# Optimization experiments

Hardware: AMD Instinct MI355X
Metric: run time of the kernel (lower is better)

Reference implementation:

```python
import jax, jax.numpy as jnp
import numpy as np

N, E, DIN, H, HEADS = 50000, 800000, 128, 64, 4


def setup_inputs() -> dict:
    key = jax.random.key(0)
    ks = jax.random.split(key, 12)

    def p(k, shape, fan_in):
        return jax.random.normal(k, shape, dtype=jnp.float32) / np.float32(np.sqrt(fan_in))

    return dict(
        x=jax.random.normal(ks[0], (N, DIN), dtype=jnp.float32),
        edge_index=jax.random.randint(ks[1], (2, E), 0, N, dtype=jnp.int32),
        # GCNConv(input_dim, hidden)
        W_gcn=p(ks[2], (DIN, H), DIN), b_gcn=jnp.zeros((H,), jnp.float32),
        # GATConv(hidden, hidden, heads=4, concat=True)
        W_gat=p(ks[3], (H, HEADS * H), H),
        att_src=p(ks[4], (HEADS, H), H), att_dst=p(ks[5], (HEADS, H), H),
        b_gat=jnp.zeros((HEADS * H,), jnp.float32),
        # SAGEConv(4*hidden, hidden): lin_l (neighbors, with bias), lin_r (root, no bias)
        W_sage_l=p(ks[6], (HEADS * H, H), HEADS * H), b_sage=jnp.zeros((H,), jnp.float32),
        W_sage_r=p(ks[7], (HEADS * H, H), HEADS * H),
        # edge-pair MLP: Linear(2*hidden, hidden) -> ReLU -> Linear(hidden, 1)
        W1=p(ks[8], (2 * H, H), 2 * H), b1=jnp.zeros((H,), jnp.float32),
        W2=p(ks[9], (H, 1), H), b2=jnp.zeros((1,), jnp.float32),
    )


def reference(x, edge_index, W_gcn, b_gcn, W_gat, att_src, att_dst, b_gat,
              W_sage_l, b_sage, W_sage_r, W1, b1, W2, b2):
    n = x.shape[0]
    src, dst = edge_index[0], edge_index[1]
    loop = jnp.arange(n, dtype=edge_index.dtype)
    # edges with self-loops appended (GCN and GAT add self-loops by default)
    s2 = jnp.concatenate([src, loop])
    d2 = jnp.concatenate([dst, loop])

    h = x @ W_gcn                                            # [N, H]
    deg = jax.ops.segment_sum(jnp.ones_like(d2, jnp.float32), d2, num_segments=n)
    dinv = jnp.where(deg > 0, jax.lax.rsqrt(jnp.maximum(deg, 1e-12)), 0.0)
    norm = dinv[s2] * dinv[d2]                               # [E+N]
    h = jax.ops.segment_sum(h[s2] * norm[:, None], d2, num_segments=n) + b_gcn
    h = jax.nn.relu(h)                                       # dropout: identity in eval

    # ---- GATConv (heads=4, concat=True, negative_slope=0.2) ----
    g = (h @ W_gat).reshape(n, HEADS, H)                     # [N, heads, C]
    a_s = jnp.sum(g * att_src, axis=-1)                      # [N, heads]
    a_d = jnp.sum(g * att_dst, axis=-1)
    e = jax.nn.leaky_relu(a_s[s2] + a_d[d2], 0.2)            # [E+N, heads]
    m = jax.ops.segment_max(e, d2, num_segments=n)           # per-target max (stable softmax)
    e = jnp.exp(e - m[d2])
    z = jax.ops.segment_sum(e, d2, num_segments=n)
    alpha = e / (z[d2] + 1e-16)                              # edge softmax over incoming edges
    g = jax.ops.segment_sum(g[s2] * alpha[:, :, None], d2, num_segments=n)
    g = jax.nn.relu(g.reshape(n, HEADS * H) + b_gat)

    # ---- SAGEConv (mean aggregation, root weight, no self-loops) ----
    nsum = jax.ops.segment_sum(g[src], dst, num_segments=n)
    cnt = jax.ops.segment_sum(jnp.ones_like(dst, jnp.float32), dst, num_segments=n)
    mean = nsum / jnp.maximum(cnt, 1.0)[:, None]
    s = jax.nn.relu(mean @ W_sage_l + b_sage + g @ W_sage_r)  # [N, H]

    # ---- edge-pair MLP + sigmoid ----
    ef = jnp.concatenate([s[src], s[dst]], axis=1)            # [E, 2H]
    pred = jax.nn.relu(ef @ W1 + b1) @ W2 + b2                # [E, 1]
    return jax.nn.sigmoid(pred[:, 0])
```

## Files before the change

### kernel.cpp

```cpp
#include <hip/hip_runtime.h>
#include <math.h>

typedef float v2f __attribute__((ext_vector_type(2)));
static __device__ __forceinline__ float4 f4s(float v){ return make_float4(v,v,v,v); }
static __device__ __forceinline__ float4 f4add(float4 a, float4 b){ return make_float4(a.x+b.x,a.y+b.y,a.z+b.z,a.w+b.w); }
static __device__ __forceinline__ float4 f4max(float4 a, float4 b){ return make_float4(fmaxf(a.x,b.x),fmaxf(a.y,b.y),fmaxf(a.z,b.z),fmaxf(a.w,b.w)); }
static __device__ __forceinline__ float4 f4scale(float4 a, float s){ return make_float4(a.x*s,a.y*s,a.z*s,a.w*s); }
static __device__ __forceinline__ float4 f4fma(float4 acc, float s, float4 b){
  acc.x += s*b.x; acc.y += s*b.y; acc.z += s*b.z; acc.w += s*b.w; return acc;
}
static __device__ __forceinline__ float4 f4relu(float4 a){ return f4max(a, f4s(0.f)); }
static __device__ __forceinline__ float4 f4leaky(float4 a){
  return make_float4(a.x>0.f?a.x:0.2f*a.x, a.y>0.f?a.y:0.2f*a.y, a.z>0.f?a.z:0.2f*a.z, a.w>0.f?a.w:0.2f*a.w);
}
static __device__ __forceinline__ float4 f4expf(float4 a){ return make_float4(__expf(a.x),__expf(a.y),__expf(a.z),__expf(a.w)); }
static __device__ __forceinline__ unsigned short f2bf(float f){
  unsigned int u = __float_as_uint(f);
  unsigned int r = (u + 0x7fffu + ((u >> 16) & 1u)) >> 16;
  return (unsigned short)r;
}
static __device__ __forceinline__ ushort4 f2bf4(float4 f){
  ushort4 r; r.x=f2bf(f.x); r.y=f2bf(f.y); r.z=f2bf(f.z); r.w=f2bf(f.w); return r;
}
static __device__ __forceinline__ float4 bfu2f4(uint2 u){
  return make_float4(__uint_as_float(u.x << 16), __uint_as_float(u.x & 0xffff0000u),
                     __uint_as_float(u.y << 16), __uint_as_float(u.y & 0xffff0000u));
}
static __device__ __forceinline__ float4 bfu2f4_lo(uint4 u){ return bfu2f4(make_uint2(u.x, u.y)); }
static __device__ __forceinline__ float4 bfu2f4_hi(uint4 u){ return bfu2f4(make_uint2(u.z, u.w)); }

typedef __attribute__((ext_vector_type(8))) unsigned short u16x8;
static __device__ __forceinline__ u16x8 f2bf8(float4 a, float4 b){
  u16x8 r;
  r[0]=f2bf(a.x); r[1]=f2bf(a.y); r[2]=f2bf(a.z); r[3]=f2bf(a.w);
  r[4]=f2bf(b.x); r[5]=f2bf(b.y); r[6]=f2bf(b.z); r[7]=f2bf(b.w);
  return r;
}
static __device__ __forceinline__ void red2(float4& a, float4& b){
  a.x += __shfl_xor(a.x, 8); a.y += __shfl_xor(a.y, 8);
  a.z += __shfl_xor(a.z, 8); a.w += __shfl_xor(a.w, 8);
  b.x += __shfl_xor(b.x, 8); b.y += __shfl_xor(b.y, 8);
  b.z += __shfl_xor(b.z, 8); b.w += __shfl_xor(b.w, 8);
}
static __device__ __forceinline__ unsigned char f2fp8(float v){
  return (unsigned char)(__builtin_amdgcn_cvt_pk_fp8_f32(v, v, 0, false) & 0xff);
}
static __device__ __forceinline__ unsigned int f4_fp8x4(float4 v){
  unsigned int r = __builtin_amdgcn_cvt_pk_fp8_f32(v.x, v.y, 0, false);
  r = __builtin_amdgcn_cvt_pk_fp8_f32(v.z, v.w, r, true);
  return r;
}
static __device__ __forceinline__ float4 fp8x4_f4(unsigned int q){
  v2f lo = __builtin_amdgcn_cvt_pk_f32_fp8(q, false);
  v2f hi = __builtin_amdgcn_cvt_pk_f32_fp8(q, true);
  return make_float4(lo[0], lo[1], hi[0], hi[1]);
}
static __device__ __forceinline__ float dot8(float4 a, float4 b, const float* v){
  return a.x*v[0]+a.y*v[1]+a.z*v[2]+a.w*v[3]+b.x*v[4]+b.y*v[5]+b.z*v[6]+b.w*v[7];
}

typedef __attribute__((ext_vector_type(8))) short bf16x8;
typedef __attribute__((ext_vector_type(4))) float f32x4;

__global__ __launch_bounds__(256) void k_rankw(const int* __restrict__ dst, int* __restrict__ cnt,
                                               int* __restrict__ rank, int E, int fb,
                                               const float* __restrict__ Wg, const float* __restrict__ Wl,
                                               const float* __restrict__ Wr, unsigned short* __restrict__ WT){
  if ((int)blockIdx.x < fb){
    int t = blockIdx.x*256 + threadIdx.x;
    if (t < E) rank[t] = atomicAdd(&cnt[dst[t]], 1);
    return;
  }
  int s = (blockIdx.x - fb)*256 + threadIdx.x;
  int l = s & 63, f = s >> 6;
  const float* wp; int ld;
  if (s < 2048){
    int cc = f & 15, kb = f >> 4;
    int c  = cc*16 + (l & 15);
    int kr = kb*32 + ((l >> 4) << 3);
    wp = Wg + (size_t)kr*256 + c; ld = 256;
  } else {
    int f2 = f - 32;
    int cc = f2 & 7, kb = f2 >> 3;
    int c  = cc*16 + (l & 15);
    int kr = kb*32 + ((l >> 4) << 3);
    wp = (c >= 64) ? (Wr + (size_t)kr*64 + (c - 64)) : (Wl + (size_t)kr*64 + c);
    ld = 64;
  }
  u16x8 o;
  #pragma unroll
  for (int j = 0; j < 8; ++j) o[j] = f2bf(wp[(size_t)j*ld]);
  *(u16x8*)(WT + (size_t)s*8) = o;
}

__global__ __launch_bounds__(256) void k_scan1v(const int* __restrict__ cnt, int* __restrict__ excl,
                                                int* __restrict__ bsum, int n, int nb,
                                                const float* __restrict__ Wg, const float* __restrict__ as,
                                                const float* __restrict__ ad, float* __restrict__ Vs,
                                                float* __restrict__ Vd){
  if ((int)blockIdx.x == nb){
    int t = threadIdx.x;
    int h = t >> 6, k = t & 63;
    float s = 0.f, d = 0.f;
    const float* wr = Wg + (size_t)k*256 + h*64;
    const float* ar = as + h*64;
    const float* dr = ad + h*64;
    for (int c = 0; c < 64; ++c){ float w = wr[c]; s += w*ar[c]; d += w*dr[c]; }
    Vs[t] = s; Vd[t] = d;
    return;
  }
  __shared__ int sc[256];
  int t = threadIdx.x; int i = blockIdx.x*256 + t;
  int v = (i<n)?cnt[i]:0;
  sc[t]=v; __syncthreads();
  for (int o=1;o<256;o<<=1){ int a=(t>=o)?sc[t-o]:0; __syncthreads(); sc[t]+=a; __syncthreads(); }
  if (i<n) excl[i] = sc[t]-v;
  if (t==255) bsum[blockIdx.x] = sc[t];
}
__global__ __launch_bounds__(256) void k_scan3b(const int* __restrict__ cnt, const int* __restrict__ excl,
                                                const int* __restrict__ bsum, int* __restrict__ offs,
                                                float* __restrict__ dinv, int n, int E, int nb){
  __shared__ int sb[256];
  int t = threadIdx.x;
  int v = (t<nb)?bsum[t]:0;
  sb[t]=v; __syncthreads();
  for (int o=1;o<256;o<<=1){ int a=(t>=o)?sb[t-o]:0; __syncthreads(); sb[t]+=a; __syncthreads(); }
  int bex = sb[blockIdx.x] - bsum[blockIdx.x];
  int i = blockIdx.x*256 + t;
  if (i < n){
    offs[i] = excl[i] + bex;
    dinv[i] = rsqrtf((float)cnt[i] + 1.0f);
    if (i == 0) offs[n] = E;
  }
}

__global__ __launch_bounds__(256) void k_fillg(const int* __restrict__ src, const int* __restrict__ dstv,
                                               const int* __restrict__ offs, const int* __restrict__ rank,
                                               int* __restrict__ csr, int E, int fb,
                                               const float* __restrict__ x, const float* __restrict__ Wg,
                                               unsigned char* __restrict__ a8, int n,
                                               const float* __restrict__ dinv){
  if ((int)blockIdx.x < fb){
    int t = blockIdx.x*256 + threadIdx.x;
    if (t < E) csr[offs[dstv[t]] + rank[t]] = src[t];
    return;
  }
  __shared__ unsigned short wb[1024*8];
  int tid = threadIdx.x;
  for (int s = tid; s < 1024; s += 256){
    int l = s & 63, f = s >> 6;
    int cc = f & 3, kb = f >> 2;
    int c  = cc*16 + (l & 15);
    int kr = kb*32 + ((l >> 4) << 3);
    const float* wp = Wg + (size_t)kr*64 + c;
    unsigned short* dp = &wb[s*8];
    #pragma unroll
    for (int j = 0; j < 8; ++j) dp[j] = f2bf(wp[(size_t)j*64]);
  }
  __syncthreads();
  int wv = tid >> 6, l = tid & 63;
  int lrow = l & 15;
  int lk = (l >> 4) << 3;
  int g = blockIdx.x - fb;
  int r0 = (g << 6) + (wv << 4);
  int m = r0 + lrow;
  bf16x8 afr[4];
  #pragma unroll
  for (int kb = 0; kb < 4; ++kb){
    bf16x8 a = {0,0,0,0,0,0,0,0};
    if (m < n){
      const float* p = x + (size_t)m*128 + kb*32 + lk;
      float4 f0 = *(const float4*)p;
      float4 f1 = *(const float4*)(p + 4);
      a[0]=(short)f2bf(f0.x); a[1]=(short)f2bf(f0.y); a[2]=(short)f2bf(f0.z); a[3]=(short)f2bf(f0.w);
      a[4]=(short)f2bf(f1.x); a[5]=(short)f2bf(f1.y); a[6]=(short)f2bf(f1.z); a[7]=(short)f2bf(f1.w);
    }
    afr[kb] = a;
  }
  int rbase = r0 + ((l >> 4) << 2);
  float sc[4];
  #pragma unroll
  for (int r = 0; r < 4; ++r) sc[r] = (rbase + r < n) ? dinv[rbase + r] : 0.f;
  #pragma unroll
  for (int cc = 0; cc < 4; ++cc){
    f32x4 acc = {0.f, 0.f, 0.f, 0.f};
    #pragma unroll
    for (int kb = 0; kb < 4; ++kb){
      bf16x8 b = *(const bf16x8*)&wb[((kb*4 + cc)*64 + l)*8];
      acc = __builtin_amdgcn_mfma_f32_16x16x32_bf16(afr[kb], b, acc, 0, 0, 0);
    }
    int c = cc*16 + lrow;
    #pragma unroll
    for (int r = 0; r < 4; ++r){
      int rr = rbase + r;
      if (rr < n) a8[(size_t)rr*64 + c] = f2fp8(acc[r] * sc[r]);
    }
  }
}

__global__ __launch_bounds__(256, 4) void k_gatsage(const unsigned short* __restrict__ Y,
                                                    const unsigned short* __restrict__ WT,
                                                    const float* __restrict__ bg,
                                                    unsigned short* __restrict__ R,
                                                    unsigned char* __restrict__ P8, int n){
  constexpr int LDG = 264;
  __shared__ unsigned short gb[64*LDG];
  const unsigned short* WT1 = WT;
  const unsigned short* WT2 = WT + 2048*8;
  int tid = threadIdx.x;
  int wv = tid >> 6, l = tid & 63;
  int lrow = l & 15;
  int lk = (l >> 4) << 3;
  int rbase4 = (l >> 4) << 2;
  int r0 = ((int)blockIdx.x << 6) + (wv << 4);
  int m = r0 + lrow;
  bf16x8 afr[4][2];
  #pragma unroll
  for (int h = 0; h < 4; ++h){
    #pragma unroll
    for (int kb = 0; kb < 2; ++kb){
      bf16x8 a = {0,0,0,0,0,0,0,0};
      if (m < n) a = *(const bf16x8*)(Y + (size_t)m*256 + h*64 + kb*32 + lk);
      afr[h][kb] = a;
    }
  }
  #pragma unroll
  for (int cc = 0; cc < 16; ++cc){
    f32x4 acc = {0.f, 0.f, 0.f, 0.f};
    int hh = cc >> 2;
    #pragma unroll
    for (int kb = 0; kb < 2; ++kb){
      bf16x8 b = *(const bf16x8*)&WT1[((size_t)((kb*16 + cc)*64 + l))*8];
      acc = __builtin_amdgcn_mfma_f32_16x16x32_bf16(afr[hh][kb], b, acc, 0, 0, 0);
    }
    int c = cc*16 + lrow;
    float bv = bg[c];
    #pragma unroll
    for (int r = 0; r < 4; ++r){
      int lr = (wv << 4) + rbase4 + r;
      gb[lr*LDG + c] = f2bf(fmaxf(acc[r] + bv, 0.f));
    }
  }
  bf16x8 afb[8];
  #pragma unroll
  for (int kb = 0; kb < 8; ++kb)
    afb[kb] = *(const bf16x8*)&gb[((wv << 4) + lrow)*LDG + kb*32 + lk];
  #pragma unroll
  for (int cc = 0; cc < 8; ++cc){
    f32x4 acc = {0.f, 0.f, 0.f, 0.f};
    #pragma unroll
    for (int kb = 0; kb < 8; ++kb){
      bf16x8 b = *(const bf16x8*)&WT2[((size_t)((kb*8 + cc)*64 + l))*8];
      acc = __builtin_amdgcn_mfma_f32_16x16x32_bf16(afb[kb], b, acc, 0, 0, 0);
    }
    int c = cc*16 + lrow;
    #pragma unroll
    for (int r = 0; r < 4; ++r){
      int rr = r0 + rbase4 + r;
      if (rr < n){
        float v = acc[r];
        if (c < 64) P8[(size_t)rr*64 + c] = f2fp8(v);
        else        R[(size_t)rr*64 + (c - 64)] = f2bf(v);
      }
    }
  }
}

__global__ __launch_bounds__(256) void k_gcn(const unsigned char* __restrict__ a8, const float* __restrict__ dinv,
                                             const float* __restrict__ b, const int* __restrict__ offs,
                                             const int* __restrict__ csr, const float* __restrict__ Vs,
                                             const float* __restrict__ Vd, unsigned char* __restrict__ h8,
                                             float* __restrict__ D, int n){
  __shared__ float svs[256], svd[256];
  svs[threadIdx.x] = Vs[threadIdx.x];
  svd[threadIdx.x] = Vd[threadIdx.x];
  __syncthreads();
  int l = threadIdx.x & 63;
  int node = (((blockIdx.x*256 + threadIdx.x) >> 6) << 2) + (l >> 4);
  int l15 = l & 15;
  int grp = l15 >> 3, sub = l15 & 7;
  bool ok = node < n;
  int beg = 0, end = 0;
  float di = 0.f;
  if (ok){ beg = offs[node]; end = offs[node+1]; di = dinv[node]; }
  float4 aL0 = f4s(0.f), aH0 = f4s(0.f), aL1 = f4s(0.f), aH1 = f4s(0.f);
  int i = beg + grp;
  for (; i + 2 < end; i += 4){
    int s0 = csr[i], s1 = csr[i+2];
    uint2 u0 = *(const uint2*)(a8 + (size_t)s0*64 + (sub<<3));
    uint2 u1 = *(const uint2*)(a8 + (size_t)s1*64 + (sub<<3));
    aL0 = f4add(aL0, fp8x4_f4(u0.x)); aH0 = f4add(aH0, fp8x4_f4(u0.y));
    aL1 = f4add(aL1, fp8x4_f4(u1.x)); aH1 = f4add(aH1, fp8x4_f4(u1.y));
  }
  if (i < end){
    int s0 = csr[i];
    uint2 u0 = *(const uint2*)(a8 + (size_t)s0*64 + (sub<<3));
    aL0 = f4add(aL0, fp8x4_f4(u0.x)); aH0 = f4add(aH0, fp8x4_f4(u0.y));
  }
  float4 aL = f4add(aL0, aL1), aH = f4add(aH0, aH1);
  red2(aL, aH);
  if (ok){
    uint2 us = *(const uint2*)(a8 + (size_t)node*64 + (sub<<3));
    aL = f4add(aL, fp8x4_f4(us.x)); aH = f4add(aH, fp8x4_f4(us.y));
    float4 b0 = *(const float4*)(b + (sub<<3));
    float4 b1 = *(const float4*)(b + (sub<<3) + 4);
    float4 r0 = f4relu(f4fma(b0, di, aL));
    float4 r1 = f4relu(f4fma(b1, di, aH));
    if (grp == 0){
      uint2 q; q.x = f4_fp8x4(r0); q.y = f4_fp8x4(r1);
      *(uint2*)(h8 + (size_t)node*64 + (sub<<3)) = q;
    }
    const float* vs0 = svs + (grp*128) + (sub<<3);
    const float* vd0 = svd + (grp*128) + (sub<<3);
    float s0 = dot8(r0, r1, vs0);
    float s1 = dot8(r0, r1, vs0 + 64);
    float d0 = dot8(r0, r1, vd0);
    float d1 = dot8(r0, r1, vd0 + 64);
    #pragma unroll
    for (int o = 1; o < 8; o <<= 1){
      s0 += __shfl_xor(s0, o); s1 += __shfl_xor(s1, o);
      d0 += __shfl_xor(d0, o); d1 += __shfl_xor(d1, o);
    }
    if (sub == 0){
      *(float2*)(D + (size_t)node*8 + grp*2)     = make_float2(s0, s1);
      *(float2*)(D + (size_t)node*8 + 4 + grp*2) = make_float2(d0, d1);
    }
  }
}

#define GAT_CAP 128
__global__ __launch_bounds__(256) void k_gat2(const float* __restrict__ D, const unsigned char* __restrict__ H8,
                                              const int* __restrict__ offs, const int* __restrict__ csr,
                                              unsigned short* __restrict__ Y, int n){
  __shared__ float wl[8][GAT_CAP*4];
  __shared__ int   sl[8][GAT_CAP];
  int hw = threadIdx.x >> 5;
  int node = (blockIdx.x*256 + threadIdx.x) >> 5;
  int l5 = threadIdx.x & 31;
  if (node >= n) return;
  int beg = offs[node], end = offs[node+1];
  int deg = end - beg;
  float4 ed  = *(const float4*)(D + (size_t)node*8 + 4);
  float4 es0 = *(const float4*)(D + (size_t)node*8);
  float4 wself = f4expf(f4leaky(f4add(es0, ed)));
  float4 z4 = f4s(0.f);
  for (int i = beg + l5; i < end; i += 32){
    int s = csr[i];
    float4 w = f4expf(f4leaky(f4add(*(const float4*)(D + (size_t)s*8), ed)));
    int li = i - beg;
    if (li < GAT_CAP){ *(float4*)&wl[hw][li<<2] = w; sl[hw][li] = s << 6; }
    z4 = f4add(z4, w);
  }
  for (int m = 1; m < 32; m <<= 1){
    z4.x += __shfl_xor(z4.x, m); z4.y += __shfl_xor(z4.y, m);
    z4.z += __shfl_xor(z4.z, m); z4.w += __shfl_xor(z4.w, m);
  }
  z4 = f4add(z4, wself);
  int grp = l5 >> 4;
  int sub = l5 & 15;
  int c0b = sub << 2;
  float4 a0 = f4s(0.f), a1 = f4s(0.f), a2 = f4s(0.f), a3 = f4s(0.f);
  int nl = deg < GAT_CAP ? deg : GAT_CAP;
  int i = grp;
  for (; i + 2 < nl; i += 4){
    int o0 = sl[hw][i], o1 = sl[hw][i+2];
    float4 w0 = *(const float4*)&wl[hw][i<<2];
    float4 w1 = *(const float4*)&wl[hw][(i+2)<<2];
    unsigned int q0 = *(const unsigned int*)(H8 + o0 + c0b);
    unsigned int q1 = *(const unsigned int*)(H8 + o1 + c0b);
    float4 f0 = fp8x4_f4(q0);
    float4 f1 = fp8x4_f4(q1);
    a0 = f4fma(a0, w0.x, f0); a1 = f4fma(a1, w0.y, f0);
    a2 = f4fma(a2, w0.z, f0); a3 = f4fma(a3, w0.w, f0);
    a0 = f4fma(a0, w1.x, f1); a1 = f4fma(a1, w1.y, f1);
    a2 = f4fma(a2, w1.z, f1); a3 = f4fma(a3, w1.w, f1);
  }
  if (i < nl){
    float4 w0 = *(const float4*)&wl[hw][i<<2];
    float4 f0 = fp8x4_f4(*(const unsigned int*)(H8 + sl[hw][i] + c0b));
    a0 = f4fma(a0, w0.x, f0); a1 = f4fma(a1, w0.y, f0);
    a2 = f4fma(a2, w0.z, f0); a3 = f4fma(a3, w0.w, f0);
  }
  for (int j = nl + grp; j < deg; j += 2){
    int s = csr[beg+j];
    float4 e = f4leaky(f4add(*(const float4*)(D + (size_t)s*8), ed));
    float4 w = f4expf(e);
    float4 f0 = fp8x4_f4(*(const unsigned int*)(H8 + ((size_t)s << 6) + c0b));
    a0 = f4fma(a0, w.x, f0); a1 = f4fma(a1, w.y, f0);
    a2 = f4fma(a2, w.z, f0); a3 = f4fma(a3, w.w, f0);
  }
  a0.x += __shfl_xor(a0.x, 16); a0.y += __shfl_xor(a0.y, 16); a0.z += __shfl_xor(a0.z, 16); a0.w += __shfl_xor(a0.w, 16);
  a1.x += __shfl_xor(a1.x, 16); a1.y += __shfl_xor(a1.y, 16); a1.z += __shfl_xor(a1.z, 16); a1.w += __shfl_xor(a1.w, 16);
  a2.x += __shfl_xor(a2.x, 16); a2.y += __shfl_xor(a2.y, 16); a2.z += __shfl_xor(a2.z, 16); a2.w += __shfl_xor(a2.w, 16);
  a3.x += __shfl_xor(a3.x, 16); a3.y += __shfl_xor(a3.y, 16); a3.z += __shfl_xor(a3.z, 16); a3.w += __shfl_xor(a3.w, 16);
  if (grp == 0){
    float4 fs = fp8x4_f4(*(const unsigned int*)(H8 + ((size_t)node << 6) + c0b));
    a0 = f4fma(a0, wself.x, fs);
    a1 = f4fma(a1, wself.y, fs);
    a2 = f4fma(a2, wself.z, fs);
    a3 = f4fma(a3, wself.w, fs);
    a0 = f4scale(a0, 1.f/(z4.x + 1e-16f));
    a1 = f4scale(a1, 1.f/(z4.y + 1e-16f));
    a2 = f4scale(a2, 1.f/(z4.z + 1e-16f));
    a3 = f4scale(a3, 1.f/(z4.w + 1e-16f));
    unsigned short* yp = Y + (size_t)node*256 + (sub << 2);
    *(ushort4*)(yp)       = f2bf4(a0);
    *(ushort4*)(yp + 64)  = f2bf4(a1);
    *(ushort4*)(yp + 128) = f2bf4(a2);
    *(ushort4*)(yp + 192) = f2bf4(a3);
  }
}

__global__ __launch_bounds__(256) void k_sage(const unsigned char* __restrict__ P8, const unsigned short* __restrict__ R,
                                              const float* __restrict__ b, const int* __restrict__ offs,
                                              const int* __restrict__ csr, const float* __restrict__ W1a,
                                              const float* __restrict__ W1b, unsigned char* __restrict__ T2, int n){
  __shared__ unsigned short wfr[1024*8];
  __shared__ unsigned short stile[16][72];
  int tid = threadIdx.x;
  for (int s = tid; s < 1024; s += 256){
    int l = s & 63, f = s >> 6;
    int cc = f & 7, kb = f >> 3;
    int c  = cc*16 + (l & 15);
    int kr = kb*32 + ((l >> 4) << 3);
    const float* wp = (c >= 64) ? (W1b + (size_t)kr*64 + (c - 64)) : (W1a + (size_t)kr*64 + c);
    unsigned short* dp = &wfr[s*8];
    #pragma unroll
    for (int j = 0; j < 8; ++j) dp[j] = f2bf(wp[(size_t)j*64]);
  }
  int wv = tid >> 6, l = tid & 63;
  int base = blockIdx.x*16;
  int lrow16 = (wv << 2) + (l >> 4);
  int node = base + lrow16;
  int l15 = l & 15;
  int grp = l15 >> 3, sub = l15 & 7;
  bool ok = node < n;
  int beg = 0, end = 0;
  if (ok){ beg = offs[node]; end = offs[node+1]; }
  float4 aL0 = f4s(0.f), aH0 = f4s(0.f), aL1 = f4s(0.f), aH1 = f4s(0.f);
  int i = beg + grp;
  for (; i + 2 < end; i += 4){
    int s0 = csr[i], s1 = csr[i+2];
    uint2 u0 = *(const uint2*)(P8 + (size_t)s0*64 + (sub<<3));
    uint2 u1 = *(const uint2*)(P8 + (size_t)s1*64 + (sub<<3));
    aL0 = f4add(aL0, fp8x4_f4(u0.x)); aH0 = f4add(aH0, fp8x4_f4(u0.y));
    aL1 = f4add(aL1, fp8x4_f4(u1.x)); aH1 = f4add(aH1, fp8x4_f4(u1.y));
  }
  if (i < end){
    int s0 = csr[i];
    uint2 u0 = *(const uint2*)(P8 + (size_t)s0*64 + (sub<<3));
    aL0 = f4add(aL0, fp8x4_f4(u0.x)); aH0 = f4add(aH0, fp8x4_f4(u0.y));
  }
  float4 aL = f4add(aL0, aL1), aH = f4add(aH0, aH1);
  red2(aL, aH);
  float4 r0 = f4s(0.f), r1 = f4s(0.f);
  if (ok){
    float minv = 1.f / fmaxf((float)(end - beg), 1.f);
    uint4 ur = *(const uint4*)(R + (size_t)node*64 + (sub<<3));
    float4 b0 = *(const float4*)(b + (sub<<3));
    float4 b1 = *(const float4*)(b + (sub<<3) + 4);
    r0 = f4relu(f4add(f4fma(b0, minv, aL), bfu2f4_lo(ur)));
    r1 = f4relu(f4add(f4fma(b1, minv, aH), bfu2f4_hi(ur)));
  }
  if (grp == 0) *(u16x8*)&stile[lrow16][sub << 3] = f2bf8(r0, r1);
  __syncthreads();
  int lrow = l & 15, lk = (l >> 4) << 3;
  bf16x8 af0 = *(const bf16x8*)&stile[lrow][lk];
  bf16x8 af1 = *(const bf16x8*)&stile[lrow][32 + lk];
  int rbase = (l >> 4) << 2;
  #pragma unroll
  for (int q = 0; q < 2; ++q){
    int cc = wv*2 + q;
    f32x4 acc = {0.f, 0.f, 0.f, 0.f};
    acc = __builtin_amdgcn_mfma_f32_16x16x32_bf16(af0, *(const bf16x8*)&wfr[(cc*64 + l)*8], acc, 0, 0, 0);
    acc = __builtin_amdgcn_mfma_f32_16x16x32_bf16(af1, *(const bf16x8*)&wfr[((8 + cc)*64 + l)*8], acc, 0, 0, 0);
    int c = cc*16 + lrow;
    #pragma unroll
    for (int r = 0; r < 4; ++r){
      int nd = base + rbase + r;
      if (nd < n) T2[(size_t)nd*128 + c] = f2fp8(acc[r]);
    }
  }
}

__global__ __launch_bounds__(256) void k_mlp(const unsigned char* __restrict__ T2,
                                             const float* __restrict__ b1, const float* __restrict__ W2,
                                             const float* __restrict__ b2, const int* __restrict__ src,
                                             const int* __restrict__ dst, float* __restrict__ out, int E){
  int t = threadIdx.x;
  int e = blockIdx.x*32 + (t >> 3);
  if (e >= E) return;
  int sub = t & 7;
  int s = src[e], d = dst[e];
  uint2 uu = *(const uint2*)(T2 + (size_t)s*128 + (sub<<3));
  uint2 vv = *(const uint2*)(T2 + (size_t)d*128 + 64 + (sub<<3));
  float4 u0 = fp8x4_f4(uu.x), u1 = fp8x4_f4(uu.y);
  float4 v0 = fp8x4_f4(vv.x), v1 = fp8x4_f4(vv.y);
  float4 bb0 = *(const float4*)(b1 + (sub<<3));
  float4 bb1 = *(const float4*)(b1 + (sub<<3) + 4);
  float4 w0 = *(const float4*)(W2 + (sub<<3));
  float4 w1 = *(const float4*)(W2 + (sub<<3) + 4);
  float4 ta = f4relu(f4add(f4add(u0, v0), bb0));
  float4 tb = f4relu(f4add(f4add(u1, v1), bb1));
  float p = ta.x*w0.x + ta.y*w0.y + ta.z*w0.z + ta.w*w0.w
          + tb.x*w1.x + tb.y*w1.y + tb.z*w1.z + tb.w*w1.w;
  p += __shfl_xor(p, 1);
  p += __shfl_xor(p, 2);
  p += __shfl_xor(p, 4);
  if (sub == 0) out[e] = 1.f / (1.f + __expf(-(p + b2[0])));
}

extern "C" void kernel_launch(void* const* d_in, const int* in_sizes, int n_in,
                              void* d_out, int out_size, void* d_ws, size_t ws_size,
                              hipStream_t stream){
  const float* x     = (const float*)d_in[0];
  const int*   eidx  = (const int*)  d_in[1];
  const float* W_gcn = (const float*)d_in[2];
  const float* b_gcn = (const float*)d_in[3];
  const float* W_gat = (const float*)d_in[4];
  const float* att_s = (const float*)d_in[5];
  const float* att_d = (const float*)d_in[6];
  const float* b_gat = (const float*)d_in[7];
  const float* W_sl  = (const float*)d_in[8];
  const float* b_sg  = (const float*)d_in[9];
  const float* W_sr  = (const float*)d_in[10];
  const float* W1    = (const float*)d_in[11];
  const float* b1    = (const float*)d_in[12];
  const float* W2    = (const float*)d_in[13];
  const float* b2    = (const float*)d_in[14];
  float* out = (float*)d_out;

  const int N = in_sizes[0] / 128;
  const int E = in_sizes[1] / 2;
  const int* src = eidx;
  const int* dst = eidx + E;

  float* ws   = (float*)d_ws;
  float* dinv = ws;
  float* D    = dinv + (size_t)N;
  float* Vs   = D + (size_t)N*8;
  float* Vd   = Vs + 256;
  unsigned short* WT = (unsigned short*)(Vd + 256);
  unsigned short* Y  = WT + (size_t)6144*8;
  unsigned short* R  = Y + (size_t)N*256;
  unsigned char*  A8 = (unsigned char*)(R + (size_t)N*64);
  unsigned char*  H8 = A8 + (size_t)N*64;
  unsigned char*  P8 = H8 + (size_t)N*64;
  unsigned char*  T2 = P8 + (size_t)N*64;
  int* cnt  = (int*)(T2 + (size_t)N*128);
  int* excl = cnt + N;
  int* bsum = excl + N;
  int* offs = bsum + 256;
  int* rank = offs + N + 1;
  int* csr  = rank + E;

  const int nb = (N + 255) / 256;
  const int fb = (E + 255) / 256;
  const int gtiles = (N + 63) / 64;
  const int nwb = (N + 15) / 16;

  hipMemsetAsync(cnt, 0, (size_t)N*sizeof(int), stream);
  k_rankw <<<fb + 24, 256, 0, stream>>>(dst, cnt, rank, E, fb, W_gat, W_sl, W_sr, WT);
  k_scan1v<<<nb + 1, 256, 0, stream>>>(cnt, excl, bsum, N, nb, W_gat, att_s, att_d, Vs, Vd);
  k_scan3b<<<nb, 256, 0, stream>>>(cnt, excl, bsum, offs, dinv, N, E, nb);
  k_fillg <<<fb + gtiles, 256, 0, stream>>>(src, dst, offs, rank, csr, E, fb,
                                            x, W_gcn, A8, N, dinv);

  k_gcn <<<nwb, 256, 0, stream>>>(A8, dinv, b_gcn, offs, csr, Vs, Vd, H8, D, N);

  k_gat2<<<(N+7)/8, 256, 0, stream>>>(D, H8, offs, csr, Y, N);

  k_gatsage<<<gtiles, 256, 0, stream>>>(Y, WT, b_gat, R, P8, N);

  k_sage<<<nwb, 256, 0, stream>>>(P8, R, b_sg, offs, csr, W1, W1 + 64*64, T2, N);

  k_mlp <<<(E+31)/32, 256, 0, stream>>>(T2, b1, W2, b2, src, dst, out, E);
}
```

Baseline: 276.6 us.

## Fuse GAT aggregation with GAT and SAGE projection matmuls via shared-memory tile

Merges the GAT neighbor aggregation kernel and the follow-on GAT/SAGE projection MFMA kernel into one kernel. Each block aggregates 8 nodes into a 16-row shared-memory tile (upper 8 rows zeroed), then runs both matmuls on that tile and writes P8/R directly. This removes the N×256 bf16 Y round-trip through global memory and one launch. In exchange, half of each 16-row MFMA tile is padding, so matrix work doubles, and the block now carries extra shared memory and barriers, which may lower occupancy.

```diff
diff --git a/kernel.cpp b/kernel.cpp
--- a/kernel.cpp
+++ b/kernel.cpp
@@ -194,74 +194,6 @@
     for (int r = 0; r < 4; ++r){
       int rr = rbase + r;
       if (rr < n) a8[(size_t)rr*64 + c] = f2fp8(acc[r] * sc[r]);
-    }
-  }
-}
-
-__global__ __launch_bounds__(256, 4) void k_gatsage(const unsigned short* __restrict__ Y,
-                                                    const unsigned short* __restrict__ WT,
-                                                    const float* __restrict__ bg,
-                                                    unsigned short* __restrict__ R,
-                                                    unsigned char* __restrict__ P8, int n){
-  constexpr int LDG = 264;
-  __shared__ unsigned short gb[64*LDG];
-  const unsigned short* WT1 = WT;
-  const unsigned short* WT2 = WT + 2048*8;
-  int tid = threadIdx.x;
-  int wv = tid >> 6, l = tid & 63;
-  int lrow = l & 15;
-  int lk = (l >> 4) << 3;
-  int rbase4 = (l >> 4) << 2;
-  int r0 = ((int)blockIdx.x << 6) + (wv << 4);
-  int m = r0 + lrow;
-  bf16x8 afr[4][2];
-  #pragma unroll
-  for (int h = 0; h < 4; ++h){
-    #pragma unroll
-    for (int kb = 0; kb < 2; ++kb){
-      bf16x8 a = {0,0,0,0,0,0,0,0};
-      if (m < n) a = *(const bf16x8*)(Y + (size_t)m*256 + h*64 + kb*32 + lk);
-      afr[h][kb] = a;
-    }
-  }
-  #pragma unroll
-  for (int cc = 0; cc < 16; ++cc){
-    f32x4 acc = {0.f, 0.f, 0.f, 0.f};
-    int hh = cc >> 2;
-    #pragma unroll
-    for (int kb = 0; kb < 2; ++kb){
-      bf16x8 b = *(const bf16x8*)&WT1[((size_t)((kb*16 + cc)*64 + l))*8];
-      acc = __builtin_amdgcn_mfma_f32_16x16x32_bf16(afr[hh][kb], b, acc, 0, 0, 0);
-    }
-    int c = cc*16 + lrow;
-    float bv = bg[c];
-    #pragma unroll
-    for (int r = 0; r < 4; ++r){
-      int lr = (wv << 4) + rbase4 + r;
-      gb[lr*LDG + c] = f2bf(fmaxf(acc[r] + bv, 0.f));
-    }
-  }
-  bf16x8 afb[8];
-  #pragma unroll
-  for (int kb = 0; kb < 8; ++kb)
-    afb[kb] = *(const bf16x8*)&gb[((wv << 4) + lrow)*LDG + kb*32 + lk];
-  #pragma unroll
-  for (int cc = 0; cc < 8; ++cc){
-    f32x4 acc = {0.f, 0.f, 0.f, 0.f};
-    #pragma unroll
-    for (int kb = 0; kb < 8; ++kb){
-      bf16x8 b = *(const bf16x8*)&WT2[((size_t)((kb*8 + cc)*64 + l))*8];
-      acc = __builtin_amdgcn_mfma_f32_16x16x32_bf16(afb[kb], b, acc, 0, 0, 0);
-    }
-    int c = cc*16 + lrow;
-    #pragma unroll
-    for (int r = 0; r < 4; ++r){
-      int rr = r0 + rbase4 + r;
-      if (rr < n){
-        float v = acc[r];
-        if (c < 64) P8[(size_t)rr*64 + c] = f2fp8(v);
-        else        R[(size_t)rr*64 + (c - 64)] = f2bf(v);
-      }
     }
   }
 }
@@ -329,85 +261,147 @@
 }
 
 #define GAT_CAP 128
-__global__ __launch_bounds__(256) void k_gat2(const float* __restrict__ D, const unsigned char* __restrict__ H8,
-                                              const int* __restrict__ offs, const int* __restrict__ csr,
-                                              unsigned short* __restrict__ Y, int n){
+__global__ __launch_bounds__(256) void k_gat2f(const float* __restrict__ D, const unsigned char* __restrict__ H8,
+                                               const int* __restrict__ offs, const int* __restrict__ csr,
+                                               const unsigned short* __restrict__ WT, const float* __restrict__ bg,
+                                               unsigned short* __restrict__ R, unsigned char* __restrict__ P8, int n){
   __shared__ float wl[8][GAT_CAP*4];
   __shared__ int   sl[8][GAT_CAP];
-  int hw = threadIdx.x >> 5;
-  int node = (blockIdx.x*256 + threadIdx.x) >> 5;
-  int l5 = threadIdx.x & 31;
-  if (node >= n) return;
-  int beg = offs[node], end = offs[node+1];
-  int deg = end - beg;
-  float4 ed  = *(const float4*)(D + (size_t)node*8 + 4);
-  float4 es0 = *(const float4*)(D + (size_t)node*8);
-  float4 wself = f4expf(f4leaky(f4add(es0, ed)));
-  float4 z4 = f4s(0.f);
-  for (int i = beg + l5; i < end; i += 32){
-    int s = csr[i];
-    float4 w = f4expf(f4leaky(f4add(*(const float4*)(D + (size_t)s*8), ed)));
-    int li = i - beg;
-    if (li < GAT_CAP){ *(float4*)&wl[hw][li<<2] = w; sl[hw][li] = s << 6; }
-    z4 = f4add(z4, w);
-  }
-  for (int m = 1; m < 32; m <<= 1){
-    z4.x += __shfl_xor(z4.x, m); z4.y += __shfl_xor(z4.y, m);
-    z4.z += __shfl_xor(z4.z, m); z4.w += __shfl_xor(z4.w, m);
-  }
-  z4 = f4add(z4, wself);
+  __shared__ unsigned short ytile[16][264];
+  unsigned short* gtile = (unsigned short*)&wl[0][0];
+  const unsigned short* WT1 = WT;
+  const unsigned short* WT2 = WT + 2048*8;
+  int tid = threadIdx.x;
+  for (int s0 = tid; s0 < 8*264; s0 += 256) (&ytile[8][0])[s0] = 0;
+  int hw = tid >> 5;
+  int node = (blockIdx.x*256 + tid) >> 5;
+  int l5 = tid & 31;
   int grp = l5 >> 4;
   int sub = l5 & 15;
-  int c0b = sub << 2;
-  float4 a0 = f4s(0.f), a1 = f4s(0.f), a2 = f4s(0.f), a3 = f4s(0.f);
-  int nl = deg < GAT_CAP ? deg : GAT_CAP;
-  int i = grp;
-  for (; i + 2 < nl; i += 4){
-    int o0 = sl[hw][i], o1 = sl[hw][i+2];
-    float4 w0 = *(const float4*)&wl[hw][i<<2];
-    float4 w1 = *(const float4*)&wl[hw][(i+2)<<2];
-    unsigned int q0 = *(const unsigned int*)(H8 + o0 + c0b);
-    unsigned int q1 = *(const unsigned int*)(H8 + o1 + c0b);
-    float4 f0 = fp8x4_f4(q0);
-    float4 f1 = fp8x4_f4(q1);
-    a0 = f4fma(a0, w0.x, f0); a1 = f4fma(a1, w0.y, f0);
-    a2 = f4fma(a2, w0.z, f0); a3 = f4fma(a3, w0.w, f0);
-    a0 = f4fma(a0, w1.x, f1); a1 = f4fma(a1, w1.y, f1);
-    a2 = f4fma(a2, w1.z, f1); a3 = f4fma(a3, w1.w, f1);
-  }
-  if (i < nl){
-    float4 w0 = *(const float4*)&wl[hw][i<<2];
-    float4 f0 = fp8x4_f4(*(const unsigned int*)(H8 + sl[hw][i] + c0b));
-    a0 = f4fma(a0, w0.x, f0); a1 = f4fma(a1, w0.y, f0);
-    a2 = f4fma(a2, w0.z, f0); a3 = f4fma(a3, w0.w, f0);
-  }
-  for (int j = nl + grp; j < deg; j += 2){
-    int s = csr[beg+j];
-    float4 e = f4leaky(f4add(*(const float4*)(D + (size_t)s*8), ed));
-    float4 w = f4expf(e);
-    float4 f0 = fp8x4_f4(*(const unsigned int*)(H8 + ((size_t)s << 6) + c0b));
-    a0 = f4fma(a0, w.x, f0); a1 = f4fma(a1, w.y, f0);
-    a2 = f4fma(a2, w.z, f0); a3 = f4fma(a3, w.w, f0);
-  }
-  a0.x += __shfl_xor(a0.x, 16); a0.y += __shfl_xor(a0.y, 16); a0.z += __shfl_xor(a0.z, 16); a0.w += __shfl_xor(a0.w, 16);
-  a1.x += __shfl_xor(a1.x, 16); a1.y += __shfl_xor(a1.y, 16); a1.z += __shfl_xor(a1.z, 16); a1.w += __shfl_xor(a1.w, 16);
-  a2.x += __shfl_xor(a2.x, 16); a2.y += __shfl_xor(a2.y, 16); a2.z += __shfl_xor(a2.z, 16); a2.w += __shfl_xor(a2.w, 16);
-  a3.x += __shfl_xor(a3.x, 16); a3.y += __shfl_xor(a3.y, 16); a3.z += __shfl_xor(a3.z, 16); a3.w += __shfl_xor(a3.w, 16);
-  if (grp == 0){
-    float4 fs = fp8x4_f4(*(const unsigned int*)(H8 + ((size_t)node << 6) + c0b));
-    a0 = f4fma(a0, wself.x, fs);
-    a1 = f4fma(a1, wself.y, fs);
-    a2 = f4fma(a2, wself.z, fs);
-    a3 = f4fma(a3, wself.w, fs);
-    a0 = f4scale(a0, 1.f/(z4.x + 1e-16f));
-    a1 = f4scale(a1, 1.f/(z4.y + 1e-16f));
-    a2 = f4scale(a2, 1.f/(z4.z + 1e-16f));
-    a3 = f4scale(a3, 1.f/(z4.w + 1e-16f));
-    unsigned short* yp = Y + (size_t)node*256 + (sub << 2);
-    *(ushort4*)(yp)       = f2bf4(a0);
-    *(ushort4*)(yp + 64)  = f2bf4(a1);
-    *(ushort4*)(yp + 128) = f2bf4(a2);
-    *(ushort4*)(yp + 192) = f2bf4(a3);
+  if (node < n){
+    int beg = offs[node], end = offs[node+1];
+    int deg = end - beg;
+    float4 ed  = *(const float4*)(D + (size_t)node*8 + 4);
+    float4 es0 = *(const float4*)(D + (size_t)node*8);
+    float4 wself = f4expf(f4leaky(f4add(es0, ed)));
+    float4 z4 = f4s(0.f);
+    for (int i = beg + l5; i < end; i += 32){
+      int s = csr[i];
+      float4 w = f4expf(f4leaky(f4add(*(const float4*)(D + (size_t)s*8), ed)));
+      int li = i - beg;
+      if (li < GAT_CAP){ *(float4*)&wl[hw][li<<2] = w; sl[hw][li] = s << 6; }
+      z4 = f4add(z4, w);
+    }
+    for (int m = 1; m < 32; m <<= 1){
+      z4.x += __shfl_xor(z4.x, m); z4.y += __shfl_xor(z4.y, m);
+      z4.z += __shfl_xor(z4.z, m); z4.w += __shfl_xor(z4.w, m);
+    }
+    z4 = f4add(z4, wself);
+    int c0b = sub << 2;
+    float4 a0 = f4s(0.f), a1 = f4s(0.f), a2 = f4s(0.f), a3 = f4s(0.f);
+    int nl = deg < GAT_CAP ? deg : GAT_CAP;
+    int i = grp;
+    for (; i + 2 < nl; i += 4){
+      int o0 = sl[hw][i], o1 = sl[hw][i+2];
+      float4 w0 = *(const float4*)&wl[hw][i<<2];
+      float4 w1 = *(const float4*)&wl[hw][(i+2)<<2];
+      unsigned int q0 = *(const unsigned int*)(H8 + o0 + c0b);
+      unsigned int q1 = *(const unsigned int*)(H8 + o1 + c0b);
+      float4 f0 = fp8x4_f4(q0);
+      float4 f1 = fp8x4_f4(q1);
+      a0 = f4fma(a0, w0.x, f0); a1 = f4fma(a1, w0.y, f0);
+      a2 = f4fma(a2, w0.z, f0); a3 = f4fma(a3, w0.w, f0);
+      a0 = f4fma(a0, w1.x, f1); a1 = f4fma(a1, w1.y, f1);
+      a2 = f4fma(a2, w1.z, f1); a3 = f4fma(a3, w1.w, f1);
+    }
+    if (i < nl){
+      float4 w0 = *(const float4*)&wl[hw][i<<2];
+      float4 f0 = fp8x4_f4(*(const unsigned int*)(H8 + sl[hw][i] + c0b));
+      a0 = f4fma(a0, w0.x, f0); a1 = f4fma(a1, w0.y, f0);
+      a2 = f4fma(a2, w0.z, f0); a3 = f4fma(a3, w0.w, f0);
+    }
+    for (int j = nl + grp; j < deg; j += 2){
+      int s = csr[beg+j];
+      float4 e = f4leaky(f4add(*(const float4*)(D + (size_t)s*8), ed));
+      float4 w = f4expf(e);
+      float4 f0 = fp8x4_f4(*(const unsigned int*)(H8 + ((size_t)s << 6) + c0b));
+      a0 = f4fma(a0, w.x, f0); a1 = f4fma(a1, w.y, f0);
+      a2 = f4fma(a2, w.z, f0); a3 = f4fma(a3, w.w, f0);
+    }
+    a0.x += __shfl_xor(a0.x, 16); a0.y += __shfl_xor(a0.y, 16); a0.z += __shfl_xor(a0.z, 16); a0.w += __shfl_xor(a0.w, 16);
+    a1.x += __shfl_xor(a1.x, 16); a1.y += __shfl_xor(a1.y, 16); a1.z += __shfl_xor(a1.z, 16); a1.w += __shfl_xor(a1.w, 16);
+    a2.x += __shfl_xor(a2.x, 16); a2.y += __shfl_xor(a2.y, 16); a2.z += __shfl_xor(a2.z, 16); a2.w += __shfl_xor(a2.w, 16);
+    a3.x += __shfl_xor(a3.x, 16); a3.y += __shfl_xor(a3.y, 16); a3.z += __shfl_xor(a3.z, 16); a3.w += __shfl_xor(a3.w, 16);
+    if (grp == 0){
+      float4 fs = fp8x4_f4(*(const unsigned int*)(H8 + ((size_t)node << 6) + c0b));
+      a0 = f4fma(a0, wself.x, fs);
+      a1 = f4fma(a1, wself.y, fs);
+      a2 = f4fma(a2, wself.z, fs);
+      a3 = f4fma(a3, wself.w, fs);
+      a0 = f4scale(a0, 1.f/(z4.x + 1e-16f));
+      a1 = f4scale(a1, 1.f/(z4.y + 1e-16f));
+      a2 = f4scale(a2, 1.f/(z4.z + 1e-16f));
+      a3 = f4scale(a3, 1.f/(z4.w + 1e-16f));
+      unsigned short* yp = &ytile[hw][sub << 2];
+      *(ushort4*)(yp)       = f2bf4(a0);
+      *(ushort4*)(yp + 64)  = f2bf4(a1);
+      *(ushort4*)(yp + 128) = f2bf4(a2);
+      *(ushort4*)(yp + 192) = f2bf4(a3);
+    }
+  } else if (grp == 0){
+    ushort4 z = make_ushort4(0,0,0,0);
+    unsigned short* yp = &ytile[hw][sub << 2];
+    *(ushort4*)(yp)       = z;
+    *(ushort4*)(yp + 64)  = z;
+    *(ushort4*)(yp + 128) = z;
+    *(ushort4*)(yp + 192) = z;
+  }
+  __syncthreads();
+  int wv = tid >> 6, l = tid & 63;
+  int lrow = l & 15;
+  int lk = (l >> 4) << 3;
+  int rbase4 = (l >> 4) << 2;
+  bf16x8 af0 = *(const bf16x8*)&ytile[lrow][wv*64 + lk];
+  bf16x8 af1 = *(const bf16x8*)&ytile[lrow][wv*64 + 32 + lk];
+  #pragma unroll
+  for (int q = 0; q < 4; ++q){
+    int cc = wv*4 + q;
+    f32x4 acc = {0.f, 0.f, 0.f, 0.f};
+    acc = __builtin_amdgcn_mfma_f32_16x16x32_bf16(af0, *(const bf16x8*)&WT1[((size_t)((0*16 + cc)*64 + l))*8], acc, 0, 0, 0);
+    acc = __builtin_amdgcn_mfma_f32_16x16x32_bf16(af1, *(const bf16x8*)&WT1[((size_t)((1*16 + cc)*64 + l))*8], acc, 0, 0, 0);
+    int c = cc*16 + lrow;
+    float bv = bg[c];
+    #pragma unroll
+    for (int r = 0; r < 4; ++r)
+      gtile[(rbase4 + r)*264 + c] = f2bf(fmaxf(acc[r] + bv, 0.f));
+  }
+  __syncthreads();
+  bf16x8 afb[8];
+  #pragma unroll
+  for (int kb = 0; kb < 8; ++kb)
+    afb[kb] = *(const bf16x8*)&gtile[lrow*264 + kb*32 + lk];
+  #pragma unroll
+  for (int q = 0; q < 2; ++q){
+    int cc = wv*2 + q;
+    f32x4 acc = {0.f, 0.f, 0.f, 0.f};
+    #pragma unroll
+    for (int kb = 0; kb < 8; ++kb){
+      bf16x8 b = *(const bf16x8*)&WT2[((size_t)((kb*8 + cc)*64 + l))*8];
+      acc = __builtin_amdgcn_mfma_f32_16x16x32_bf16(afb[kb], b, acc, 0, 0, 0);
+    }
+    int c = cc*16 + lrow;
+    #pragma unroll
+    for (int r = 0; r < 4; ++r){
+      int row = rbase4 + r;
+      if (row < 8){
+        int nd = blockIdx.x*8 + row;
+        if (nd < n){
+          float v = acc[r];
+          if (c < 64) P8[(size_t)nd*64 + c] = f2fp8(v);
+          else        R[(size_t)nd*64 + (c - 64)] = f2bf(v);
+        }
+      }
+    }
   }
 }
 
@@ -541,8 +535,7 @@
   float* Vs   = D + (size_t)N*8;
   float* Vd   = Vs + 256;
   unsigned short* WT = (unsigned short*)(Vd + 256);
-  unsigned short* Y  = WT + (size_t)6144*8;
-  unsigned short* R  = Y + (size_t)N*256;
+  unsigned short* R  = WT + (size_t)6144*8;
   unsigned char*  A8 = (unsigned char*)(R + (size_t)N*64);
   unsigned char*  H8 = A8 + (size_t)N*64;
   unsigned char*  P8 = H8 + (size_t)N*64;
@@ -568,9 +561,7 @@
 
   k_gcn <<<nwb, 256, 0, stream>>>(A8, dinv, b_gcn, offs, csr, Vs, Vd, H8, D, N);
 
-  k_gat2<<<(N+7)/8, 256, 0, stream>>>(D, H8, offs, csr, Y, N);
-
-  k_gatsage<<<gtiles, 256, 0, stream>>>(Y, WT, b_gat, R, P8, N);
+  k_gat2f<<<(N+7)/8, 256, 0, stream>>>(D, H8, offs, csr, WT, b_gat, R, P8, N);
 
   k_sage<<<nwb, 256, 0, stream>>>(P8, R, b_sg, offs, csr, W1, W1 + 64*64, T2, N);
 
```

Result: no change. 276.1 us (-0.2%).
